# Optimization experiments

Hardware: AMD Instinct MI355X
Metric: run time of the kernel (lower is better)

The kernel has to match this reference:

```python
import jax, jax.numpy as jnp
import numpy as np

HIDDEN = 4096
NHQ = 32
NHKV = 8
HEAD_DIM = HIDDEN // NHQ  # 128
THETA = 10000.0


def _rope(x, theta_base):
    # x: [b, h, s, d]; half-split RoPE as in the torch module
    b, h, s, d = x.shape
    inv_freq = 1.0 / (theta_base ** (jnp.arange(0, d, 2, dtype=jnp.float32)[: d // 2] / d))
    freqs = jnp.arange(s, dtype=jnp.float32)[:, None] * inv_freq[None, :]  # [s, d/2]
    cos = jnp.cos(freqs).astype(x.dtype)
    sin = jnp.sin(freqs).astype(x.dtype)
    x1, x2 = x[..., : d // 2], x[..., d // 2 :]
    return jnp.concatenate([x1 * cos - x2 * sin, x2 * cos + x1 * sin], axis=-1)


def setup_inputs() -> dict:
    key = jax.random.key(0)
    ks = jax.random.split(key, 5)
    std = 1.0 / np.sqrt(HIDDEN)
    x = jax.random.normal(ks[0], (2, 2048, HIDDEN), dtype=jnp.float32)
    # weights stored as [in, out] so y = x @ W (equivalent to torch Linear with W.T)
    Wq = jax.random.normal(ks[1], (HIDDEN, HIDDEN), dtype=jnp.float32) * std
    Wk = jax.random.normal(ks[2], (HIDDEN, NHKV * HEAD_DIM), dtype=jnp.float32) * std
    Wv = jax.random.normal(ks[3], (HIDDEN, NHKV * HEAD_DIM), dtype=jnp.float32) * std
    Wo = jax.random.normal(ks[4], (HIDDEN, HIDDEN), dtype=jnp.float32) * std
    return {"x": x, "Wq": Wq, "Wk": Wk, "Wv": Wv, "Wo": Wo}


def reference(x, Wq, Wk, Wv, Wo):
    b, s, _ = x.shape
    q_per_kv = NHQ // NHKV
    # projections -> [b, h, s, d]
    q = (x @ Wq).reshape(b, s, NHQ, HEAD_DIM).transpose(0, 2, 1, 3)
    k = (x @ Wk).reshape(b, s, NHKV, HEAD_DIM).transpose(0, 2, 1, 3)
    v = (x @ Wv).reshape(b, s, NHKV, HEAD_DIM).transpose(0, 2, 1, 3)
    q = _rope(q, THETA)
    k = _rope(k, THETA)
    # GQA: group q heads by kv head instead of repeat_interleaving K/V.
    # torch repeat_interleave maps q head h -> kv head h // q_per_kv,
    # matching this [b, kv, q_per_kv, s, d] grouping.
    qg = q.reshape(b, NHKV, q_per_kv, s, HEAD_DIM)
    scores = jnp.einsum("bkgqd,bkmd->bkgqm", qg, k) / np.sqrt(HEAD_DIM)
    causal = jnp.tril(jnp.ones((s, s), dtype=bool))
    scores = jnp.where(causal, scores, -jnp.inf)
    attn = jax.nn.softmax(scores, axis=-1)
    out = jnp.einsum("bkgqm,bkmd->bkgqd", attn, v)  # [b, kv, g, s, d]
    out = out.reshape(b, NHQ, s, HEAD_DIM).transpose(0, 2, 1, 3).reshape(b, s, HIDDEN)
    return out @ Wo
```

## Files before the change

### kernel.cpp

```cpp
#include <hip/hip_runtime.h>
#include <hip/hip_bf16.h>
#include <math.h>

typedef __bf16  bf16x8 __attribute__((ext_vector_type(8)));
typedef __bf16  bf16x4 __attribute__((ext_vector_type(4)));
typedef __bf16  bf16x2 __attribute__((ext_vector_type(2)));
typedef float   f32x4  __attribute__((ext_vector_type(4)));
typedef unsigned int uint32;

#define HIDDEN 4096
#define NHQ    32
#define NHKV   8
#define HD     128
#define SEQ    2048
#define BATCH  2
#define NTOK   (BATCH * SEQ)
#define KVDIM  (NHKV * HD)

#define MBYTE  (1024ull * 1024ull)

__device__ inline void load8(const float* p, __bf16* d)
{
    float4 a = *reinterpret_cast<const float4*>(p);
    float4 b = *reinterpret_cast<const float4*>(p + 4);
    d[0] = (__bf16)a.x; d[1] = (__bf16)a.y; d[2] = (__bf16)a.z; d[3] = (__bf16)a.w;
    d[4] = (__bf16)b.x; d[5] = (__bf16)b.y; d[6] = (__bf16)b.z; d[7] = (__bf16)b.w;
}
__device__ inline void load8(const __hip_bfloat16* p, __bf16* d)
{
    *reinterpret_cast<bf16x8*>(d) = *reinterpret_cast<const bf16x8*>(p);
}

__device__ inline void storeC(float* C, size_t idx, float v)          { C[idx] = v; }
__device__ inline void storeC(__hip_bfloat16* C, size_t idx, float v) { C[idx] = __float2bfloat16(v); }

__global__ __launch_bounds__(256) void cast_f2b(
    const float* __restrict__ in, __hip_bfloat16* __restrict__ out, size_t n8)
{
    size_t i = (size_t)blockIdx.x * blockDim.x + threadIdx.x;
    if (i >= n8) return;
    const float* p = in + i * 8;
    float4 a = *reinterpret_cast<const float4*>(p);
    float4 b = *reinterpret_cast<const float4*>(p + 4);
    bf16x8 v;
    v[0] = (__bf16)a.x; v[1] = (__bf16)a.y; v[2] = (__bf16)a.z; v[3] = (__bf16)a.w;
    v[4] = (__bf16)b.x; v[5] = (__bf16)b.y; v[6] = (__bf16)b.z; v[7] = (__bf16)b.w;
    *reinterpret_cast<bf16x8*>(out + i * 8) = v;
}

__global__ __launch_bounds__(256) void transpose_cast(
    const float* __restrict__ W, int ldw,
    __hip_bfloat16* __restrict__ Wt, int K)
{
    __shared__ __align__(16) float tf[32][36];
    const int k0 = blockIdx.x * 32;
    const int n0 = blockIdx.y * 32;
    const int r  = threadIdx.x >> 3;
    const int c4 = (threadIdx.x & 7) * 4;

    *reinterpret_cast<float4*>(&tf[r][c4]) =
        *reinterpret_cast<const float4*>(W + (size_t)(k0 + r) * ldw + n0 + c4);
    __syncthreads();

    bf16x4 o;
    o[0] = (__bf16)tf[c4 + 0][r]; o[1] = (__bf16)tf[c4 + 1][r];
    o[2] = (__bf16)tf[c4 + 2][r]; o[3] = (__bf16)tf[c4 + 3][r];
    *reinterpret_cast<bf16x4*>(Wt + (size_t)(n0 + r) * K + k0 + c4) = o;
}

#define GBM 128
#define GBN 128
#define GBK 32

template <typename TC>
__global__ __launch_bounds__(256) void gemm128r(
    const __hip_bfloat16* __restrict__ A,
    const __hip_bfloat16* __restrict__ Bt,
    TC* __restrict__ C,
    int M, int N, int K, int ldc)
{
    __shared__ __align__(16) __bf16 As[GBM][GBK];
    __shared__ __align__(16) __bf16 Bs[GBN][GBK];

    const int tid  = threadIdx.x;
    const int w    = tid >> 6;
    const int lane = tid & 63;
    const int lrow = lane & 15;
    const int lq   = lane >> 4;
    const int bm   = blockIdx.y * GBM;
    const int bn   = blockIdx.x * GBN;
    const int wr   = (w >> 1) * 64;
    const int wc   = (w & 1) * 64;

    const int srow = tid >> 1;
    const int scol = (tid & 1) * 16;

    f32x4 acc[4][4] = {};

    const __hip_bfloat16* ga = A  + (size_t)(bm + srow) * K + scol;
    const __hip_bfloat16* gb = Bt + (size_t)(bn + srow) * K + scol;

    for (int k0 = 0; k0 < K; k0 += GBK) {
        bf16x8 a0 = *reinterpret_cast<const bf16x8*>(ga + k0);
        bf16x8 a1 = *reinterpret_cast<const bf16x8*>(ga + k0 + 8);
        bf16x8 b0 = *reinterpret_cast<const bf16x8*>(gb + k0);
        bf16x8 b1 = *reinterpret_cast<const bf16x8*>(gb + k0 + 8);

        *reinterpret_cast<bf16x8*>(&As[srow][scol])     = a0;
        *reinterpret_cast<bf16x8*>(&As[srow][scol + 8]) = a1;
        *reinterpret_cast<bf16x8*>(&Bs[srow][scol])     = b0;
        *reinterpret_cast<bf16x8*>(&Bs[srow][scol + 8]) = b1;

        __syncthreads();

        bf16x8 af[4], bfr[4];
        #pragma unroll
        for (int i = 0; i < 4; ++i) {
            af[i]  = *reinterpret_cast<const bf16x8*>(&As[wr + i * 16 + lrow][lq * 8]);
            bfr[i] = *reinterpret_cast<const bf16x8*>(&Bs[wc + i * 16 + lrow][lq * 8]);
        }
        #pragma unroll
        for (int mi = 0; mi < 4; ++mi)
            #pragma unroll
            for (int ni = 0; ni < 4; ++ni)
                acc[mi][ni] = __builtin_amdgcn_mfma_f32_16x16x32_bf16(
                    af[mi], bfr[ni], acc[mi][ni], 0, 0, 0);

        __syncthreads();
    }

    #pragma unroll
    for (int mi = 0; mi < 4; ++mi)
        #pragma unroll
        for (int ni = 0; ni < 4; ++ni)
            #pragma unroll
            for (int r = 0; r < 4; ++r) {
                int row = bm + wr + mi * 16 + lq * 4 + r;
                int col = bn + wc + ni * 16 + lrow;
                storeC(C, (size_t)row * ldc + col, acc[mi][ni][r]);
            }
}

#define BM 64
#define BN 64
#define BK 32
#define LDSS 40

template <typename TA, typename TB, typename TC>
__global__ __launch_bounds__(256) void gemm_to(
    const TA* __restrict__ A,
    const TB* __restrict__ B,
    TC* __restrict__ C,
    int M, int N, int K)
{
    __shared__ __align__(16) __bf16 As[BM][LDSS];
    __shared__ __align__(16) __bf16 Bs[BN][LDSS];

    const int tid  = threadIdx.x;
    const int bm   = blockIdx.y * BM;
    const int bn   = blockIdx.x * BN;
    const int wave = tid >> 6;
    const int lane = tid & 63;
    const int wr   = (wave >> 1) * 32;
    const int wc   = (wave & 1) * 32;
    const int lrow = lane & 15;
    const int lq   = lane >> 4;

    f32x4 acc[2][2] = {};

    const int ar = tid >> 2;
    const int ac = (tid & 3) * 8;
    const int br = tid >> 3;
    const int bc = (tid & 7) * 8;

    for (int k0 = 0; k0 < K; k0 += BK) {
        __bf16 abuf[8], bbuf[8];
        load8(A + (size_t)(bm + ar) * K + (k0 + ac), abuf);
        load8(B + (size_t)(k0 + br) * N + (bn + bc), bbuf);

        *reinterpret_cast<bf16x8*>(&As[ar][ac]) = *reinterpret_cast<bf16x8*>(abuf);
        #pragma unroll
        for (int j = 0; j < 8; ++j)
            Bs[bc + j][br] = bbuf[j];

        __syncthreads();

        bf16x8 afrag[2], bfrag[2];
        #pragma unroll
        for (int mi = 0; mi < 2; ++mi)
            afrag[mi] = *reinterpret_cast<const bf16x8*>(&As[wr + mi * 16 + lrow][lq * 8]);
        #pragma unroll
        for (int ni = 0; ni < 2; ++ni)
            bfrag[ni] = *reinterpret_cast<const bf16x8*>(&Bs[wc + ni * 16 + lrow][lq * 8]);

        #pragma unroll
        for (int mi = 0; mi < 2; ++mi)
            #pragma unroll
            for (int ni = 0; ni < 2; ++ni)
                acc[mi][ni] = __builtin_amdgcn_mfma_f32_16x16x32_bf16(
                    afrag[mi], bfrag[ni], acc[mi][ni], 0, 0, 0);

        __syncthreads();
    }

    #pragma unroll
    for (int mi = 0; mi < 2; ++mi)
        #pragma unroll
        for (int ni = 0; ni < 2; ++ni)
            #pragma unroll
            for (int r = 0; r < 4; ++r) {
                int row = bm + wr + mi * 16 + lq * 4 + r;
                int col = bn + wc + ni * 16 + lrow;
                storeC(C, (size_t)row * N + col, acc[mi][ni][r]);
            }
}

__global__ __launch_bounds__(256) void rope_kernel(
    __hip_bfloat16* __restrict__ X, int nh, size_t total)
{
    size_t idx = (size_t)blockIdx.x * blockDim.x + threadIdx.x;
    if (idx >= total) return;
    int    i   = (int)(idx & 63);
    size_t t   = idx >> 6;
    int    h   = (int)(t % nh);
    size_t tok = t / nh;
    int    pos = (int)(tok & (SEQ - 1));

    float inv_freq = exp2f(-(float)i * (13.287712379549449f / 64.0f));
    float fr = (float)pos * inv_freq;
    float sv, cv;
    sincosf(fr, &sv, &cv);

    size_t base = tok * ((size_t)nh * HD) + (size_t)h * HD + i;
    float x1 = __bfloat162float(X[base]);
    float x2 = __bfloat162float(X[base + 64]);
    X[base]      = __float2bfloat16(x1 * cv - x2 * sv);
    X[base + 64] = __float2bfloat16(x2 * cv + x1 * sv);
}

__global__ __launch_bounds__(256) void transpose_v(
    const __hip_bfloat16* __restrict__ Vb,
    __hip_bfloat16* __restrict__ Vt)
{
    __shared__ __align__(16) __bf16 t[32][36];
    const int bz = blockIdx.z;
    const int s0 = blockIdx.x * 32;
    const int c0 = blockIdx.y * 32;
    const int r  = threadIdx.x >> 3;
    const int c4 = (threadIdx.x & 7) * 4;

    *reinterpret_cast<bf16x4*>(&t[r][c4]) =
        *reinterpret_cast<const bf16x4*>(Vb + ((size_t)bz * SEQ + s0 + r) * KVDIM + c0 + c4);
    __syncthreads();

    bf16x4 o;
    o[0] = t[c4 + 0][r]; o[1] = t[c4 + 1][r];
    o[2] = t[c4 + 2][r]; o[3] = t[c4 + 3][r];
    *reinterpret_cast<bf16x4*>(Vt + ((size_t)bz * KVDIM + c0 + r) * SEQ + s0 + c4) = o;
}

__global__ __launch_bounds__(256) void attn_mfma(
    const __hip_bfloat16* __restrict__ Qg,
    const __hip_bfloat16* __restrict__ Kg,
    const __hip_bfloat16* __restrict__ Vt,
    __hip_bfloat16* __restrict__ Og)
{
    __shared__ __align__(16) __bf16 Pl[4][32][40];
    __shared__ __align__(16) __bf16 Ol[4][16][136];

    const int wv   = threadIdx.x >> 6;
    const int lane = threadIdx.x & 63;
    const int lq   = lane & 15;
    const int g    = lane >> 4;

    const int bid = blockIdx.x;
    const int khb = (bid & 7) * 2 + ((bid >> 3) & 1);
    const int j   = bid >> 4;
    const int qt  = (j & 1) ? (j >> 1) : (63 - (j >> 1));
    const int b   = khb >> 3;
    const int kh  = khb & 7;
    const int qh  = kh * 4 + wv;
    const int q0  = qt * 32;

    bf16x8 qf[2][4];
#pragma unroll
    for (int h = 0; h < 2; ++h) {
        const __hip_bfloat16* qrow =
            Qg + ((size_t)b * SEQ + q0 + h * 16 + lq) * HIDDEN + (size_t)qh * HD;
#pragma unroll
        for (int dj = 0; dj < 4; ++dj)
            qf[h][dj] = *reinterpret_cast<const bf16x8*>(qrow + dj * 32 + g * 8);
    }

    const __hip_bfloat16* Kb = Kg + ((size_t)b * SEQ) * KVDIM + (size_t)kh * HD;
    const __hip_bfloat16* Vb = Vt + ((size_t)b * KVDIM + (size_t)kh * HD) * SEQ;

    f32x4 oacc0[8] = {};
    f32x4 oacc1[8] = {};
    float m_run[2] = { -INFINITY, -INFINITY };
    float l_run[2] = { 0.0f, 0.0f };
    const float SCALE = 0.08838834764831845f;

    const int kv_len = q0 + 32;
    for (int k0 = 0; k0 < kv_len; k0 += 32) {
        bf16x8 kreg[8];
#pragma unroll
        for (int kt = 0; kt < 2; ++kt)
#pragma unroll
            for (int dj = 0; dj < 4; ++dj)
                kreg[kt * 4 + dj] = *reinterpret_cast<const bf16x8*>(
                    Kb + (size_t)(k0 + kt * 16 + lq) * KVDIM + dj * 32 + g * 8);

        f32x4 sacc[2][2] = {};
        __builtin_amdgcn_s_setprio(1);
#pragma unroll
        for (int kt = 0; kt < 2; ++kt)
#pragma unroll
            for (int dj = 0; dj < 4; ++dj) {
                sacc[0][kt] = __builtin_amdgcn_mfma_f32_16x16x32_bf16(
                    kreg[kt * 4 + dj], qf[0][dj], sacc[0][kt], 0, 0, 0);
                sacc[1][kt] = __builtin_amdgcn_mfma_f32_16x16x32_bf16(
                    kreg[kt * 4 + dj], qf[1][dj], sacc[1][kt], 0, 0, 0);
            }
        __builtin_amdgcn_s_setprio(0);

        bf16x8 vreg[8];
#pragma unroll
        for (int dt = 0; dt < 8; ++dt)
            vreg[dt] = *reinterpret_cast<const bf16x8*>(
                Vb + (size_t)(dt * 16 + lq) * SEQ + k0 + 8 * g);

        float corr[2];
#pragma unroll
        for (int h = 0; h < 2; ++h) {
            const int q_g = q0 + h * 16 + lq;
            float p[2][4];
            float tmax = -INFINITY;
#pragma unroll
            for (int kt = 0; kt < 2; ++kt)
#pragma unroll
                for (int r = 0; r < 4; ++r) {
                    int   k_g = k0 + kt * 16 + 4 * g + r;
                    float s   = sacc[h][kt][r] * SCALE;
                    s = (k_g <= q_g) ? s : -INFINITY;
                    p[kt][r] = s;
                    tmax = fmaxf(tmax, s);
                }
            tmax = fmaxf(tmax, __shfl_xor(tmax, 16));
            tmax = fmaxf(tmax, __shfl_xor(tmax, 32));

            float m_new = fmaxf(m_run[h], tmax);
            corr[h] = __expf(m_run[h] - m_new);
            float tsum = 0.0f;
#pragma unroll
            for (int kt = 0; kt < 2; ++kt)
#pragma unroll
                for (int r = 0; r < 4; ++r) {
                    float e = __expf(p[kt][r] - m_new);
                    p[kt][r] = e;
                    tsum += e;
                }

#pragma unroll
            for (int kt = 0; kt < 2; ++kt) {
                bf16x2 lo, hi;
                lo[0] = (__bf16)p[kt][0]; lo[1] = (__bf16)p[kt][1];
                hi[0] = (__bf16)p[kt][2]; hi[1] = (__bf16)p[kt][3];
                *reinterpret_cast<bf16x2*>(&Pl[wv][h * 16 + lq][kt * 16 + 4 * g])     = lo;
                *reinterpret_cast<bf16x2*>(&Pl[wv][h * 16 + lq][kt * 16 + 4 * g + 2]) = hi;
            }

            tsum += __shfl_xor(tsum, 16);
            tsum += __shfl_xor(tsum, 32);
            l_run[h] = l_run[h] * corr[h] + tsum;
            m_run[h] = m_new;
        }

        bf16x8 pf0 = *reinterpret_cast<const bf16x8*>(&Pl[wv][lq][8 * g]);
        bf16x8 pf1 = *reinterpret_cast<const bf16x8*>(&Pl[wv][16 + lq][8 * g]);

#pragma unroll
        for (int dt = 0; dt < 8; ++dt) {
            oacc0[dt][0] *= corr[0]; oacc0[dt][1] *= corr[0];
            oacc0[dt][2] *= corr[0]; oacc0[dt][3] *= corr[0];
            oacc1[dt][0] *= corr[1]; oacc1[dt][1] *= corr[1];
            oacc1[dt][2] *= corr[1]; oacc1[dt][3] *= corr[1];
        }
        __builtin_amdgcn_s_setprio(1);
#pragma unroll
        for (int dt = 0; dt < 8; ++dt) {
            oacc0[dt] = __builtin_amdgcn_mfma_f32_16x16x32_bf16(vreg[dt], pf0, oacc0[dt], 0, 0, 0);
            oacc1[dt] = __builtin_amdgcn_mfma_f32_16x16x32_bf16(vreg[dt], pf1, oacc1[dt], 0, 0, 0);
        }
        __builtin_amdgcn_s_setprio(0);
    }

#pragma unroll
    for (int h = 0; h < 2; ++h) {
        const f32x4* oa = h ? oacc1 : oacc0;
        float inv = 1.0f / l_run[h];
#pragma unroll
        for (int dt = 0; dt < 8; ++dt) {
            bf16x2 lo, hi;
            lo[0] = (__bf16)(oa[dt][0] * inv); lo[1] = (__bf16)(oa[dt][1] * inv);
            hi[0] = (__bf16)(oa[dt][2] * inv); hi[1] = (__bf16)(oa[dt][3] * inv);
            *reinterpret_cast<bf16x2*>(&Ol[wv][lq][dt * 16 + 4 * g])     = lo;
            *reinterpret_cast<bf16x2*>(&Ol[wv][lq][dt * 16 + 4 * g + 2]) = hi;
        }

        __hip_bfloat16* orow =
            Og + ((size_t)b * SEQ + q0 + h * 16 + lq) * HIDDEN + (size_t)qh * HD;
#pragma unroll
        for (int jj = 0; jj < 4; ++jj) {
            int c = jj * 4 + g;
            bf16x8 v = *reinterpret_cast<const bf16x8*>(&Ol[wv][lq][c * 8]);
            *reinterpret_cast<bf16x8*>(orow + c * 8) = v;
        }
    }
}

extern "C" void kernel_launch(void* const* d_in, const int* in_sizes, int n_in,
                              void* d_out, int out_size, void* d_ws, size_t ws_size,
                              hipStream_t stream)
{
    const float* x  = (const float*)d_in[0];
    const float* Wq = (const float*)d_in[1];
    const float* Wk = (const float*)d_in[2];
    const float* Wv = (const float*)d_in[3];
    const float* Wo = (const float*)d_in[4];
    float* out = (float*)d_out;

    char* ws = (char*)d_ws;
    dim3 blk(256);

    if (ws_size >= 112 * MBYTE) {
        __hip_bfloat16* Qb = (__hip_bfloat16*)(ws +  0 * MBYTE);
        __hip_bfloat16* Kb = (__hip_bfloat16*)(ws + 32 * MBYTE);
        __hip_bfloat16* Vb = (__hip_bfloat16*)(ws + 40 * MBYTE);
        __hip_bfloat16* xb = (__hip_bfloat16*)(ws + 48 * MBYTE);
        __hip_bfloat16* Vt = (__hip_bfloat16*)(ws + 48 * MBYTE);
        __hip_bfloat16* Wt = (__hip_bfloat16*)(ws + 80 * MBYTE);

        cast_f2b<<<(NTOK * HIDDEN / 8 + 255) / 256, blk, 0, stream>>>(
            x, xb, (size_t)NTOK * HIDDEN / 8);

        transpose_cast<<<dim3(HIDDEN / 32, HIDDEN / 32), blk, 0, stream>>>(Wq, HIDDEN, Wt, HIDDEN);
        gemm128r<__hip_bfloat16><<<dim3(HIDDEN / GBN, NTOK / GBM), blk, 0, stream>>>(
            xb, Wt, Qb, NTOK, HIDDEN, HIDDEN, HIDDEN);

        transpose_cast<<<dim3(HIDDEN / 32, KVDIM / 32), blk, 0, stream>>>(Wk, KVDIM, Wt, HIDDEN);
        gemm128r<__hip_bfloat16><<<dim3(KVDIM / GBN, NTOK / GBM), blk, 0, stream>>>(
            xb, Wt, Kb, NTOK, KVDIM, HIDDEN, KVDIM);

        transpose_cast<<<dim3(HIDDEN / 32, KVDIM / 32), blk, 0, stream>>>(Wv, KVDIM, Wt, HIDDEN);
        gemm128r<__hip_bfloat16><<<dim3(KVDIM / GBN, NTOK / GBM), blk, 0, stream>>>(
            xb, Wt, Vb, NTOK, KVDIM, HIDDEN, KVDIM);

        {
            size_t totq = (size_t)NTOK * NHQ * 64;
            size_t totk = (size_t)NTOK * NHKV * 64;
            rope_kernel<<<(unsigned)((totq + 255) / 256), blk, 0, stream>>>(Qb, NHQ,  totq);
            rope_kernel<<<(unsigned)((totk + 255) / 256), blk, 0, stream>>>(Kb, NHKV, totk);
        }

        transpose_v<<<dim3(SEQ / 32, KVDIM / 32, BATCH), blk, 0, stream>>>(Vb, Vt);

        attn_mfma<<<BATCH * NHKV * (SEQ / 32), blk, 0, stream>>>(Qb, Kb, Vt, Qb);

        transpose_cast<<<dim3(HIDDEN / 32, HIDDEN / 32), blk, 0, stream>>>(Wo, HIDDEN, Wt, HIDDEN);
        gemm128r<float><<<dim3(HIDDEN / GBN, NTOK / GBM), blk, 0, stream>>>(
            Qb, Wt, out, NTOK, HIDDEN, HIDDEN, HIDDEN);
    } else {
        __hip_bfloat16* Qb = (__hip_bfloat16*)ws;
        __hip_bfloat16* Kb = (__hip_bfloat16*)(ws + (size_t)NTOK * HIDDEN * 2);
        __hip_bfloat16* Vb = (__hip_bfloat16*)(ws + (size_t)NTOK * HIDDEN * 2
                                                  + (size_t)NTOK * KVDIM * 2);

        const size_t base_ws  = (size_t)NTOK * HIDDEN * 2 + 2 * (size_t)NTOK * KVDIM * 2;
        const size_t vt_bytes = (size_t)NTOK * KVDIM * 2;
        __hip_bfloat16* Vtr = (ws_size >= base_ws + vt_bytes)
                            ? (__hip_bfloat16*)(ws + base_ws)
                            : (__hip_bfloat16*)d_out;

        gemm_to<float, float, __hip_bfloat16><<<dim3(HIDDEN / BN, NTOK / BM), blk, 0, stream>>>(
            x, Wq, Qb, NTOK, HIDDEN, HIDDEN);
        gemm_to<float, float, __hip_bfloat16><<<dim3(KVDIM / BN, NTOK / BM), blk, 0, stream>>>(
            x, Wk, Kb, NTOK, KVDIM, HIDDEN);
        gemm_to<float, float, __hip_bfloat16><<<dim3(KVDIM / BN, NTOK / BM), blk, 0, stream>>>(
            x, Wv, Vb, NTOK, KVDIM, HIDDEN);

        {
            size_t totq = (size_t)NTOK * NHQ * 64;
            size_t totk = (size_t)NTOK * NHKV * 64;
            rope_kernel<<<(unsigned)((totq + 255) / 256), blk, 0, stream>>>(Qb, NHQ,  totq);
            rope_kernel<<<(unsigned)((totk + 255) / 256), blk, 0, stream>>>(Kb, NHKV, totk);
        }

        transpose_v<<<dim3(SEQ / 32, KVDIM / 32, BATCH), blk, 0, stream>>>(Vb, Vtr);

        attn_mfma<<<BATCH * NHKV * (SEQ / 32), blk, 0, stream>>>(Qb, Kb, Vtr, Qb);

        gemm_to<__hip_bfloat16, float, float><<<dim3(HIDDEN / BN, NTOK / BM), blk, 0, stream>>>(
            Qb, Wo, out, NTOK, HIDDEN, HIDDEN);
    }
}
```

Measured before the change: 1.229 ms.

## Prefetch next GEMM K-tile into registers and split attention into single-wave blocks

```diff
diff --git a/kernel.cpp b/kernel.cpp
--- a/kernel.cpp
+++ b/kernel.cpp
@@ -100,18 +100,25 @@
     const __hip_bfloat16* ga = A  + (size_t)(bm + srow) * K + scol;
     const __hip_bfloat16* gb = Bt + (size_t)(bn + srow) * K + scol;
 
+    bf16x8 pa0 = *reinterpret_cast<const bf16x8*>(ga);
+    bf16x8 pa1 = *reinterpret_cast<const bf16x8*>(ga + 8);
+    bf16x8 pb0 = *reinterpret_cast<const bf16x8*>(gb);
+    bf16x8 pb1 = *reinterpret_cast<const bf16x8*>(gb + 8);
+
     for (int k0 = 0; k0 < K; k0 += GBK) {
-        bf16x8 a0 = *reinterpret_cast<const bf16x8*>(ga + k0);
-        bf16x8 a1 = *reinterpret_cast<const bf16x8*>(ga + k0 + 8);
-        bf16x8 b0 = *reinterpret_cast<const bf16x8*>(gb + k0);
-        bf16x8 b1 = *reinterpret_cast<const bf16x8*>(gb + k0 + 8);
-
-        *reinterpret_cast<bf16x8*>(&As[srow][scol])     = a0;
-        *reinterpret_cast<bf16x8*>(&As[srow][scol + 8]) = a1;
-        *reinterpret_cast<bf16x8*>(&Bs[srow][scol])     = b0;
-        *reinterpret_cast<bf16x8*>(&Bs[srow][scol + 8]) = b1;
+        *reinterpret_cast<bf16x8*>(&As[srow][scol])     = pa0;
+        *reinterpret_cast<bf16x8*>(&As[srow][scol + 8]) = pa1;
+        *reinterpret_cast<bf16x8*>(&Bs[srow][scol])     = pb0;
+        *reinterpret_cast<bf16x8*>(&Bs[srow][scol + 8]) = pb1;
 
         __syncthreads();
+
+        if (k0 + GBK < K) {
+            pa0 = *reinterpret_cast<const bf16x8*>(ga + k0 + GBK);
+            pa1 = *reinterpret_cast<const bf16x8*>(ga + k0 + GBK + 8);
+            pb0 = *reinterpret_cast<const bf16x8*>(gb + k0 + GBK);
+            pb1 = *reinterpret_cast<const bf16x8*>(gb + k0 + GBK + 8);
+        }
 
         bf16x8 af[4], bfr[4];
         #pragma unroll
@@ -259,23 +266,23 @@
     *reinterpret_cast<bf16x4*>(Vt + ((size_t)bz * KVDIM + c0 + r) * SEQ + s0 + c4) = o;
 }
 
-__global__ __launch_bounds__(256) void attn_mfma(
+__global__ __launch_bounds__(64) void attn_mfma(
     const __hip_bfloat16* __restrict__ Qg,
     const __hip_bfloat16* __restrict__ Kg,
     const __hip_bfloat16* __restrict__ Vt,
     __hip_bfloat16* __restrict__ Og)
 {
-    __shared__ __align__(16) __bf16 Pl[4][32][40];
-    __shared__ __align__(16) __bf16 Ol[4][16][136];
-
-    const int wv   = threadIdx.x >> 6;
-    const int lane = threadIdx.x & 63;
+    __shared__ __align__(16) __bf16 Pl[32][40];
+    __shared__ __align__(16) __bf16 Ol[16][136];
+
+    const int lane = threadIdx.x;
     const int lq   = lane & 15;
     const int g    = lane >> 4;
 
     const int bid = blockIdx.x;
     const int khb = (bid & 7) * 2 + ((bid >> 3) & 1);
-    const int j   = bid >> 4;
+    const int wv  = (bid >> 4) & 3;
+    const int j   = bid >> 6;
     const int qt  = (j & 1) ? (j >> 1) : (63 - (j >> 1));
     const int b   = khb >> 3;
     const int kh  = khb & 7;
@@ -366,8 +373,8 @@
                 bf16x2 lo, hi;
                 lo[0] = (__bf16)p[kt][0]; lo[1] = (__bf16)p[kt][1];
                 hi[0] = (__bf16)p[kt][2]; hi[1] = (__bf16)p[kt][3];
-                *reinterpret_cast<bf16x2*>(&Pl[wv][h * 16 + lq][kt * 16 + 4 * g])     = lo;
-                *reinterpret_cast<bf16x2*>(&Pl[wv][h * 16 + lq][kt * 16 + 4 * g + 2]) = hi;
+                *reinterpret_cast<bf16x2*>(&Pl[h * 16 + lq][kt * 16 + 4 * g])     = lo;
+                *reinterpret_cast<bf16x2*>(&Pl[h * 16 + lq][kt * 16 + 4 * g + 2]) = hi;
             }
 
             tsum += __shfl_xor(tsum, 16);
@@ -376,8 +383,8 @@
             m_run[h] = m_new;
         }
 
-        bf16x8 pf0 = *reinterpret_cast<const bf16x8*>(&Pl[wv][lq][8 * g]);
-        bf16x8 pf1 = *reinterpret_cast<const bf16x8*>(&Pl[wv][16 + lq][8 * g]);
+        bf16x8 pf0 = *reinterpret_cast<const bf16x8*>(&Pl[lq][8 * g]);
+        bf16x8 pf1 = *reinterpret_cast<const bf16x8*>(&Pl[16 + lq][8 * g]);
 
 #pragma unroll
         for (int dt = 0; dt < 8; ++dt) {
@@ -404,8 +411,8 @@
             bf16x2 lo, hi;
             lo[0] = (__bf16)(oa[dt][0] * inv); lo[1] = (__bf16)(oa[dt][1] * inv);
             hi[0] = (__bf16)(oa[dt][2] * inv); hi[1] = (__bf16)(oa[dt][3] * inv);
-            *reinterpret_cast<bf16x2*>(&Ol[wv][lq][dt * 16 + 4 * g])     = lo;
-            *reinterpret_cast<bf16x2*>(&Ol[wv][lq][dt * 16 + 4 * g + 2]) = hi;
+            *reinterpret_cast<bf16x2*>(&Ol[lq][dt * 16 + 4 * g])     = lo;
+            *reinterpret_cast<bf16x2*>(&Ol[lq][dt * 16 + 4 * g + 2]) = hi;
         }
 
         __hip_bfloat16* orow =
@@ -413,7 +420,7 @@
 #pragma unroll
         for (int jj = 0; jj < 4; ++jj) {
             int c = jj * 4 + g;
-            bf16x8 v = *reinterpret_cast<const bf16x8*>(&Ol[wv][lq][c * 8]);
+            bf16x8 v = *reinterpret_cast<const bf16x8*>(&Ol[lq][c * 8]);
             *reinterpret_cast<bf16x8*>(orow + c * 8) = v;
         }
     }
@@ -432,6 +439,7 @@
 
     char* ws = (char*)d_ws;
     dim3 blk(256);
+    dim3 ablk(64);
 
     if (ws_size >= 112 * MBYTE) {
         __hip_bfloat16* Qb = (__hip_bfloat16*)(ws +  0 * MBYTE);
@@ -465,7 +473,7 @@
 
         transpose_v<<<dim3(SEQ / 32, KVDIM / 32, BATCH), blk, 0, stream>>>(Vb, Vt);
 
-        attn_mfma<<<BATCH * NHKV * (SEQ / 32), blk, 0, stream>>>(Qb, Kb, Vt, Qb);
+        attn_mfma<<<BATCH * NHKV * (SEQ / 32) * 4, ablk, 0, stream>>>(Qb, Kb, Vt, Qb);
 
         transpose_cast<<<dim3(HIDDEN / 32, HIDDEN / 32), blk, 0, stream>>>(Wo, HIDDEN, Wt, HIDDEN);
         gemm128r<float><<<dim3(HIDDEN / GBN, NTOK / GBM), blk, 0, stream>>>(
@@ -498,7 +506,7 @@
 
         transpose_v<<<dim3(SEQ / 32, KVDIM / 32, BATCH), blk, 0, stream>>>(Vb, Vtr);
 
-        attn_mfma<<<BATCH * NHKV * (SEQ / 32), blk, 0, stream>>>(Qb, Kb, Vtr, Qb);
+        attn_mfma<<<BATCH * NHKV * (SEQ / 32) * 4, ablk, 0, stream>>>(Qb, Kb, Vtr, Qb);
 
         gemm_to<__hip_bfloat16, float, float><<<dim3(HIDDEN / BN, NTOK / BM), blk, 0, stream>>>(
             Qb, Wo, out, NTOK, HIDDEN, HIDDEN);
```

Measured after the change: 1.061 ms. 1.16x faster.
